# Kernel tuning notes

Hardware: AMD Instinct MI355X
Metric: run time of the kernel (lower is better)

## Reference

```python
import jax, jax.numpy as jnp
import numpy as np

DT = 0.5
DX = 0.01
MU_UP = 4e-05
PAD = 3  # 7x7 kernel // 2

_LAP = np.array([[0, 0, 0, 2, 0, 0, 0],
                 [0, 0, 0, -27, 0, 0, 0],
                 [0, 0, 0, 270, 0, 0, 0],
                 [2, -27, 270, -980, 270, -27, 2],
                 [0, 0, 0, 270, 0, 0, 0],
                 [0, 0, 0, -27, 0, 0, 0],
                 [0, 0, 0, 2, 0, 0, 0]], dtype=np.float32)
LAP_W = jnp.asarray(_LAP / (DX * DX) / 180.0)[None, None]  # [1,1,7,7]


def _laplace(x):
    # x: [B,1,H,W]; circular padding then valid conv (matches padding_mode='circular')
    xp = jnp.pad(x, ((0, 0), (0, 0), (PAD, PAD), (PAD, PAD)), mode='wrap')
    return jax.lax.conv_general_dilated(xp, LAP_W, (1, 1), 'VALID',
                                        dimension_numbers=('NCHW', 'OIHW', 'NCHW'))


def setup_inputs() -> dict:
    key = jax.random.key(0)
    ks = jax.random.split(key, 7)
    h = jax.random.uniform(ks[0], (16, 2, 1024, 1024), dtype=jnp.float32)
    CA = jax.random.uniform(ks[1], (), dtype=jnp.float32) - 0.5  # ~ -rand()+0.5
    CB = jax.random.uniform(ks[2], (), dtype=jnp.float32) - 0.5
    NA = -jax.random.uniform(ks[3], (), dtype=jnp.float32)
    NB = jax.random.uniform(ks[4], (), dtype=jnp.float32)
    f = 0.1 * jax.random.uniform(ks[5], (), dtype=jnp.float32)
    k = 0.1 * jax.random.uniform(ks[6], (), dtype=jnp.float32)
    return {"h": h, "CA": CA, "CB": CB, "NA": NA, "NB": NB, "f": f, "k": k}


def reference(h, CA, CB, NA, NB, f, k):
    mu_u = MU_UP * jax.nn.sigmoid(CA)
    mu_v = MU_UP * jax.nn.sigmoid(CB)

    def f_rhs(u, v):
        uv2 = u * v * v
        f_u = mu_u * _laplace(u) + NA * uv2 + f * (1.0 - u)
        f_v = mu_v * _laplace(v) + NB * uv2 - (k + f) * v
        return f_u, f_v

    u0 = h[:, 0:1]
    v0 = h[:, 1:2]
    k1_u, k1_v = f_rhs(u0, v0)
    k2_u, k2_v = f_rhs(u0 + k1_u * (DT / 2.0), v0 + k1_v * (DT / 2.0))
    k3_u, k3_v = f_rhs(u0 + k2_u * (DT / 2.0), v0 + k2_v * (DT / 2.0))
    k4_u, k4_v = f_rhs(u0 + k3_u * DT, v0 + k3_v * DT)
    u_next = u0 + DT * (k1_u + 2.0 * k2_u + 2.0 * k3_u + k4_u) / 6.0
    v_next = v0 + DT * (k1_v + 2.0 * k2_v + 2.0 * k3_v + k4_v) / 6.0
    return jnp.concatenate((u_next, v_next), axis=1)
```

## Files before the change

kernel.cpp:

```cpp
#include <hip/hip_runtime.h>


typedef float f2 __attribute__((ext_vector_type(2)));

#define HROWS 64
#define NT    512
#define STEPS (HROWS + 24)

#define W0 ((-980.0f / 1e-4f) / 180.0f)
#define W1 ((  270.0f / 1e-4f) / 180.0f)
#define W2 (( -27.0f / 1e-4f) / 180.0f)
#define W3 ((   2.0f / 1e-4f) / 180.0f)

__device__ __forceinline__ f2 sp(float s) { f2 r; r.x = s; r.y = s; return r; }
__device__ __forceinline__ f2 pfma(float s, f2 a, f2 c) {
    return __builtin_elementwise_fma(sp(s), a, c);
}

struct Hq { f2 m2, m1, p1, p2; };

__device__ __forceinline__ Hq rdq(const f2* __restrict__ L,
                                  int xm2, int xm1, int xp1, int xp2) {
    Hq q;
    q.m2 = L[xm2]; q.m1 = L[xm1]; q.p1 = L[xp1]; q.p2 = L[xp2];
    return q;
}

__device__ __forceinline__ void evalp(const f2* __restrict__ w, const Hq& q,
                                      f2& lap, f2& ctr)
{
    ctr = w[3];
    f2 vp = pfma(W1, w[2] + w[4], pfma(W2, w[1] + w[5], sp(W3) * (w[0] + w[6])));
    f2 m1 = __builtin_shufflevector(q.m1, ctr, 1, 2);
    f2 p1 = __builtin_shufflevector(ctr, q.p1, 1, 2);
    f2 m3 = __builtin_shufflevector(q.m2, q.m1, 1, 2);
    f2 p3 = __builtin_shufflevector(q.p1, q.p2, 1, 2);
    f2 hp = pfma(W1, m1 + p1, pfma(W2, q.m1 + q.p1, sp(W3) * (m3 + p3)));
    lap = pfma(W0, ctr, hp + vp);
}

#define SH6(A)  { A[5]=A[4]; A[4]=A[3]; A[3]=A[2]; A[2]=A[1]; A[1]=A[0]; }
#define SH7(A)  { A[6]=A[5]; A[5]=A[4]; A[4]=A[3]; A[3]=A[2]; A[2]=A[1]; A[1]=A[0]; }
#define SH10(A) { A[9]=A[8]; A[8]=A[7]; A[7]=A[6]; A[6]=A[5]; A[5]=A[4]; A[4]=A[3]; A[3]=A[2]; A[2]=A[1]; A[1]=A[0]; }

__global__ __launch_bounds__(NT, 2) void rcnn_rk4_march(
    const float* __restrict__ h,
    const float* __restrict__ pCA, const float* __restrict__ pCB,
    const float* __restrict__ pNA, const float* __restrict__ pNB,
    const float* __restrict__ pf,  const float* __restrict__ pk,
    float* __restrict__ out)
{
    __shared__ f2 Su[4][4][NT], Sv[4][4][NT];

    const int tid = threadIdx.x;
    const int Y0  = blockIdx.x * HROWS;
    const int b   = blockIdx.z;

    const float NA = pNA[0], NB = pNB[0];
    const float ff = pf[0];
    const float kpf = pk[0] + pf[0];
    const float mu_u = 4e-5f / (1.0f + expf(-pCA[0]));
    const float mu_v = 4e-5f / (1.0f + expf(-pCB[0]));

    const size_t baseU = (size_t)b * 2u * 1048576u;
    const size_t baseV = baseU + 1048576u;
    const float* hU = h + baseU + 2 * tid;
    const float* hV = h + baseV + 2 * tid;
    float* oU = out + baseU + 2 * tid;
    float* oV = out + baseV + 2 * tid;

    const int xm2 = (tid - 2) & 511;
    const int xm1 = (tid - 1) & 511;
    const int xp1 = (tid + 1) & 511;
    const int xp2 = (tid + 2) & 511;

    f2 u0u[7], u0v[7];
    f2 du[6],  dv[6];
    f2 y1u[10], y1v[10];
    f2 y2u[7],  y2v[7];
    f2 y3u[7],  y3v[7];

    const f2 z = sp(0.0f);
    #pragma unroll
    for (int j = 0; j < 7; ++j) { u0u[j]=z; u0v[j]=z; y2u[j]=z; y2v[j]=z; y3u[j]=z; y3v[j]=z; }
    #pragma unroll
    for (int j = 0; j < 6; ++j) { du[j]=z; dv[j]=z; }
    #pragma unroll
    for (int j = 0; j < 10; ++j) { y1u[j]=z; y1v[j]=z; }

    f2 p0u, p0v, p1u, p1v;
    {
        int r0 = (Y0 - 12) & 1023;
        int r1 = (Y0 - 11) & 1023;
        p0u = *(const f2*)(hU + (size_t)r0 * 1024);
        p0v = *(const f2*)(hV + (size_t)r0 * 1024);
        p1u = *(const f2*)(hU + (size_t)r1 * 1024);
        p1v = *(const f2*)(hV + (size_t)r1 * 1024);
    }

#define STEP(D1, D2, D3, D4, tt)                                              \
  {                                                                           \
    const int t_ = (tt);                                                      \
    \
    Hq q1u, q1v, q2u, q2v;                                                    \
    if (D1) { q1u = rdq(&Su[0][(t_ + 1) & 3][0], xm2, xm1, xp1, xp2);         \
              q1v = rdq(&Sv[0][(t_ + 1) & 3][0], xm2, xm1, xp1, xp2); }       \
    if (D2) { q2u = rdq(&Su[1][(t_ + 2) & 3][0], xm2, xm1, xp1, xp2);         \
              q2v = rdq(&Sv[1][(t_ + 2) & 3][0], xm2, xm1, xp1, xp2); }       \
         \
    f2 cu0 = (t_ & 1) ? p1u : p0u;                                            \
    f2 cv0 = (t_ & 1) ? p1v : p0v;                                            \
    SH6(du); SH6(dv); du[0] = u0u[6]; dv[0] = u0v[6];                         \
    SH7(u0u); SH7(u0v); u0u[0] = cu0; u0v[0] = cv0;                           \
    Su[0][t_ & 3][tid] = cu0; Sv[0][t_ & 3][tid] = cv0;                       \
            \
    {                                                                         \
      int yn = (Y0 - 10 + t_) & 1023;                                         \
      f2 au = *(const f2*)(hU + (size_t)yn * 1024);                           \
      f2 av = *(const f2*)(hV + (size_t)yn * 1024);                           \
      if (t_ & 1) { p1u = au; p1v = av; } else { p0u = au; p0v = av; }        \
    }                                                                         \
    if (D1) {                                                                 \
      f2 lU, cU1, lV, cV1;                                                    \
      evalp(u0u, q1u, lU, cU1);                                               \
      evalp(u0v, q1v, lV, cV1);                                               \
      f2 uv2 = cU1 * cV1 * cV1;                                               \
      f2 kU = pfma(mu_u, lU, pfma(NA, uv2, pfma(-ff, cU1, sp(ff))));          \
      f2 kV = pfma(mu_v, lV, pfma(NB, uv2, sp(-kpf) * cV1));                  \
      f2 nu = pfma(0.25f, kU, cU1), nv = pfma(0.25f, kV, cV1);                \
      SH10(y1u); SH10(y1v); y1u[0] = nu; y1v[0] = nv;                         \
      Su[1][(t_ + 1) & 3][tid] = nu; Sv[1][(t_ + 1) & 3][tid] = nv;           \
    }                                                                         \
    Hq q3u, q3v;                                                              \
    if (D3) { q3u = rdq(&Su[2][(t_ + 3) & 3][0], xm2, xm1, xp1, xp2);         \
              q3v = rdq(&Sv[2][(t_ + 3) & 3][0], xm2, xm1, xp1, xp2); }       \
    if (D2) {                                                                 \
      f2 lU, cU2, lV, cV2;                                                    \
      evalp(y1u, q2u, lU, cU2);                                               \
      evalp(y1v, q2v, lV, cV2);                                               \
      f2 uv2 = cU2 * cV2 * cV2;                                               \
      f2 kU = pfma(mu_u, lU, pfma(NA, uv2, pfma(-ff, cU2, sp(ff))));          \
      f2 kV = pfma(mu_v, lV, pfma(NB, uv2, sp(-kpf) * cV2));                  \
      f2 nu = pfma(0.25f, kU, u0u[6]), nv = pfma(0.25f, kV, u0v[6]);          \
      SH7(y2u); SH7(y2v); y2u[0] = nu; y2v[0] = nv;                           \
      Su[2][(t_ + 2) & 3][tid] = nu; Sv[2][(t_ + 2) & 3][tid] = nv;           \
    }                                                                         \
    Hq q4u, q4v;                                                              \
    if (D4) { q4u = rdq(&Su[3][t_ & 3][0], xm2, xm1, xp1, xp2);               \
              q4v = rdq(&Sv[3][t_ & 3][0], xm2, xm1, xp1, xp2); }             \
    if (D3) {                                                                 \
      f2 lU, cU3, lV, cV3;                                                    \
      evalp(y2u, q3u, lU, cU3);                                               \
      evalp(y2v, q3v, lV, cV3);                                               \
      f2 uv2 = cU3 * cV3 * cV3;                                               \
      f2 kU = pfma(mu_u, lU, pfma(NA, uv2, pfma(-ff, cU3, sp(ff))));          \
      f2 kV = pfma(mu_v, lV, pfma(NB, uv2, sp(-kpf) * cV3));                  \
      f2 nu = pfma(0.5f, kU, du[2]), nv = pfma(0.5f, kV, dv[2]);              \
      SH7(y3u); SH7(y3v); y3u[0] = nu; y3v[0] = nv;                           \
      Su[3][(t_ + 3) & 3][tid] = nu; Sv[3][(t_ + 3) & 3][tid] = nv;           \
    }                                                                         \
    if (D4) {                                                                 \
      f2 lU, cU4, lV, cV4;                                                    \
      evalp(y3u, q4u, lU, cU4);                                               \
      evalp(y3v, q4v, lV, cV4);                                               \
      f2 uv2 = cU4 * cV4 * cV4;                                               \
      f2 kU = pfma(mu_u, lU, pfma(NA, uv2, pfma(-ff, cU4, sp(ff))));          \
      f2 kV = pfma(mu_v, lV, pfma(NB, uv2, sp(-kpf) * cV4));                  \
      f2 aU = pfma(4.0f, y1u[9], kU);                                         \
      aU = pfma(8.0f, y2u[6], aU);                                            \
      aU = pfma(4.0f, cU4, aU);                                               \
      aU = pfma(-16.0f, du[5], aU);                                           \
      f2 aV = pfma(4.0f, y1v[9], kV);                                         \
      aV = pfma(8.0f, y2v[6], aV);                                            \
      aV = pfma(4.0f, cV4, aV);                                               \
      aV = pfma(-16.0f, dv[5], aV);                                           \
      f2 oUq = pfma(0.5f / 6.0f, aU, du[5]);                                  \
      f2 oVq = pfma(0.5f / 6.0f, aV, dv[5]);                                  \
      int yS = Y0 + t_ - 24;                                                  \
      *(f2*)(oU + (size_t)yS * 1024) = oUq;                                   \
      *(f2*)(oV + (size_t)yS * 1024) = oVq;                                   \
    }                                                                         \
    asm volatile("s_waitcnt lgkmcnt(0)" ::: "memory");                        \
    __builtin_amdgcn_s_barrier();                                             \
  }

    int t = 0;
    #pragma unroll 2
    for (; t < 6;  ++t) STEP(0, 0, 0, 0, t)
    #pragma unroll 2
    for (; t < 12; ++t) STEP(1, 0, 0, 0, t)
    #pragma unroll 2
    for (; t < 18; ++t) STEP(1, 1, 0, 0, t)
    #pragma unroll 2
    for (; t < 24; ++t) STEP(1, 1, 1, 0, t)
    #pragma unroll 4
    for (; t < STEPS; ++t) STEP(1, 1, 1, 1, t)
#undef STEP
}

extern "C" void kernel_launch(void* const* d_in, const int* in_sizes, int n_in,
                              void* d_out, int out_size, void* d_ws, size_t ws_size,
                              hipStream_t stream) {
    const float* h   = (const float*)d_in[0];
    const float* pCA = (const float*)d_in[1];
    const float* pCB = (const float*)d_in[2];
    const float* pNA = (const float*)d_in[3];
    const float* pNB = (const float*)d_in[4];
    const float* pf  = (const float*)d_in[5];
    const float* pk  = (const float*)d_in[6];
    float* outp = (float*)d_out;

    dim3 grid(1024 / HROWS, 1, 16);
    dim3 block(NT);
    rcnn_rk4_march<<<grid, block, 0, stream>>>(h, pCA, pCB, pNA, pNB, pf, pk, outp);
}
```

Measured before the change: 101.8 us.

## Replace shifting register windows with ring buffers and fold RK4 accumulation early

The per-row shifting register arrays are replaced by 8-entry ring buffers indexed by a compile-time step within an 8-way manually unrolled loop, so no register moves are needed per row. The RK4 combination is partially accumulated at stage 2 into an accumulator ring, which shortens the final output arithmetic and drops the long y1 history. Warm-up steps become runtime-guarded branches inside one unrolled loop instead of separate specialised loops. This raises code size and adds runtime branch conditions in the warm-up phase.

```diff
diff --git a/kernel.cpp b/kernel.cpp
--- a/kernel.cpp
+++ b/kernel.cpp
@@ -26,11 +26,12 @@
     return q;
 }
 
-__device__ __forceinline__ void evalp(const f2* __restrict__ w, const Hq& q,
-                                      f2& lap, f2& ctr)
+__device__ __forceinline__ void evalp7(f2 w0, f2 w1, f2 w2, f2 w3, f2 w4,
+                                       f2 w5, f2 w6, const Hq& q,
+                                       f2& lap, f2& ctr)
 {
-    ctr = w[3];
-    f2 vp = pfma(W1, w[2] + w[4], pfma(W2, w[1] + w[5], sp(W3) * (w[0] + w[6])));
+    ctr = w3;
+    f2 vp = pfma(W1, w2 + w4, pfma(W2, w1 + w5, sp(W3) * (w0 + w6)));
     f2 m1 = __builtin_shufflevector(q.m1, ctr, 1, 2);
     f2 p1 = __builtin_shufflevector(ctr, q.p1, 1, 2);
     f2 m3 = __builtin_shufflevector(q.m2, q.m1, 1, 2);
@@ -38,10 +39,6 @@
     f2 hp = pfma(W1, m1 + p1, pfma(W2, q.m1 + q.p1, sp(W3) * (m3 + p3)));
     lap = pfma(W0, ctr, hp + vp);
 }
-
-#define SH6(A)  { A[5]=A[4]; A[4]=A[3]; A[3]=A[2]; A[2]=A[1]; A[1]=A[0]; }
-#define SH7(A)  { A[6]=A[5]; A[5]=A[4]; A[4]=A[3]; A[3]=A[2]; A[2]=A[1]; A[1]=A[0]; }
-#define SH10(A) { A[9]=A[8]; A[8]=A[7]; A[7]=A[6]; A[6]=A[5]; A[5]=A[4]; A[4]=A[3]; A[3]=A[2]; A[2]=A[1]; A[1]=A[0]; }
 
 __global__ __launch_bounds__(NT, 2) void rcnn_rk4_march(
     const float* __restrict__ h,
@@ -74,108 +71,114 @@
     const int xp1 = (tid + 1) & 511;
     const int xp2 = (tid + 2) & 511;
 
-    f2 u0u[7], u0v[7];
-    f2 du[6],  dv[6];
-    f2 y1u[10], y1v[10];
-    f2 y2u[7],  y2v[7];
-    f2 y3u[7],  y3v[7];
+    f2 Uu[8], Uv[8], Du[8], Dv[8];
+    f2 Y1u[8], Y1v[8], Y2u[8], Y2v[8], Y3u[8], Y3v[8];
+    f2 ACu[8], ACv[8];
 
     const f2 z = sp(0.0f);
     #pragma unroll
-    for (int j = 0; j < 7; ++j) { u0u[j]=z; u0v[j]=z; y2u[j]=z; y2v[j]=z; y3u[j]=z; y3v[j]=z; }
-    #pragma unroll
-    for (int j = 0; j < 6; ++j) { du[j]=z; dv[j]=z; }
-    #pragma unroll
-    for (int j = 0; j < 10; ++j) { y1u[j]=z; y1v[j]=z; }
-
-    f2 p0u, p0v, p1u, p1v;
+    for (int j = 0; j < 8; ++j) {
+        Uu[j]=z; Uv[j]=z; Du[j]=z; Dv[j]=z;
+        Y1u[j]=z; Y1v[j]=z; Y2u[j]=z; Y2v[j]=z; Y3u[j]=z; Y3v[j]=z;
+        ACu[j]=z; ACv[j]=z;
+    }
+
+    f2 pAu, pAv, pBu, pBv;
     {
         int r0 = (Y0 - 12) & 1023;
         int r1 = (Y0 - 11) & 1023;
-        p0u = *(const f2*)(hU + (size_t)r0 * 1024);
-        p0v = *(const f2*)(hV + (size_t)r0 * 1024);
-        p1u = *(const f2*)(hU + (size_t)r1 * 1024);
-        p1v = *(const f2*)(hV + (size_t)r1 * 1024);
-    }
-
-#define STEP(D1, D2, D3, D4, tt)                                              \
+        pAu = *(const f2*)(hU + (size_t)r0 * 1024);
+        pAv = *(const f2*)(hV + (size_t)r0 * 1024);
+        pBu = *(const f2*)(hU + (size_t)r1 * 1024);
+        pBv = *(const f2*)(hV + (size_t)r1 * 1024);
+    }
+
+#define STEP(c, G1, G2, G3, G4)                                               \
   {                                                                           \
-    const int t_ = (tt);                                                      \
-    \
-    Hq q1u, q1v, q2u, q2v;                                                    \
-    if (D1) { q1u = rdq(&Su[0][(t_ + 1) & 3][0], xm2, xm1, xp1, xp2);         \
-              q1v = rdq(&Sv[0][(t_ + 1) & 3][0], xm2, xm1, xp1, xp2); }       \
-    if (D2) { q2u = rdq(&Su[1][(t_ + 2) & 3][0], xm2, xm1, xp1, xp2);         \
-              q2v = rdq(&Sv[1][(t_ + 2) & 3][0], xm2, xm1, xp1, xp2); }       \
-         \
-    f2 cu0 = (t_ & 1) ? p1u : p0u;                                            \
-    f2 cv0 = (t_ & 1) ? p1v : p0v;                                            \
-    SH6(du); SH6(dv); du[0] = u0u[6]; dv[0] = u0v[6];                         \
-    SH7(u0u); SH7(u0v); u0u[0] = cu0; u0v[0] = cv0;                           \
-    Su[0][t_ & 3][tid] = cu0; Sv[0][t_ & 3][tid] = cv0;                       \
-            \
+    const int t_ = tb + (c);                                                  \
+        \
+                     \
+    Hq q1u, q1v, q2u, q2v, q3u, q3v, q4u, q4v;                                \
+    if (G1) { q1u = rdq(&Su[0][((c)+1)&3][0], xm2, xm1, xp1, xp2);            \
+              q1v = rdq(&Sv[0][((c)+1)&3][0], xm2, xm1, xp1, xp2); }          \
+    if (G2) { q2u = rdq(&Su[1][((c)+2)&3][0], xm2, xm1, xp1, xp2);            \
+              q2v = rdq(&Sv[1][((c)+2)&3][0], xm2, xm1, xp1, xp2); }          \
+    if (G3) { q3u = rdq(&Su[2][((c)+3)&3][0], xm2, xm1, xp1, xp2);            \
+              q3v = rdq(&Sv[2][((c)+3)&3][0], xm2, xm1, xp1, xp2); }          \
+    if (G4) { q4u = rdq(&Su[3][(c)&3][0],     xm2, xm1, xp1, xp2);            \
+              q4v = rdq(&Sv[3][(c)&3][0],     xm2, xm1, xp1, xp2); }          \
+                    \
+    Du[(c)&7] = Uu[((c)+3)&7]; Dv[(c)&7] = Uv[((c)+3)&7];                     \
+                                             \
+    f2 cu0 = ((c) & 1) ? pBu : pAu;                                           \
+    f2 cv0 = ((c) & 1) ? pBv : pAv;                                           \
+    Uu[(c)&7] = cu0; Uv[(c)&7] = cv0;                                         \
+    Su[0][(c)&3][tid] = cu0; Sv[0][(c)&3][tid] = cv0;                         \
+                                             \
     {                                                                         \
       int yn = (Y0 - 10 + t_) & 1023;                                         \
       f2 au = *(const f2*)(hU + (size_t)yn * 1024);                           \
       f2 av = *(const f2*)(hV + (size_t)yn * 1024);                           \
-      if (t_ & 1) { p1u = au; p1v = av; } else { p0u = au; p0v = av; }        \
-    }                                                                         \
-    if (D1) {                                                                 \
-      f2 lU, cU1, lV, cV1;                                                    \
-      evalp(u0u, q1u, lU, cU1);                                               \
-      evalp(u0v, q1v, lV, cV1);                                               \
-      f2 uv2 = cU1 * cV1 * cV1;                                               \
-      f2 kU = pfma(mu_u, lU, pfma(NA, uv2, pfma(-ff, cU1, sp(ff))));          \
-      f2 kV = pfma(mu_v, lV, pfma(NB, uv2, sp(-kpf) * cV1));                  \
-      f2 nu = pfma(0.25f, kU, cU1), nv = pfma(0.25f, kV, cV1);                \
-      SH10(y1u); SH10(y1v); y1u[0] = nu; y1v[0] = nv;                         \
-      Su[1][(t_ + 1) & 3][tid] = nu; Sv[1][(t_ + 1) & 3][tid] = nv;           \
-    }                                                                         \
-    Hq q3u, q3v;                                                              \
-    if (D3) { q3u = rdq(&Su[2][(t_ + 3) & 3][0], xm2, xm1, xp1, xp2);         \
-              q3v = rdq(&Sv[2][(t_ + 3) & 3][0], xm2, xm1, xp1, xp2); }       \
-    if (D2) {                                                                 \
-      f2 lU, cU2, lV, cV2;                                                    \
-      evalp(y1u, q2u, lU, cU2);                                               \
-      evalp(y1v, q2v, lV, cV2);                                               \
-      f2 uv2 = cU2 * cV2 * cV2;                                               \
-      f2 kU = pfma(mu_u, lU, pfma(NA, uv2, pfma(-ff, cU2, sp(ff))));          \
-      f2 kV = pfma(mu_v, lV, pfma(NB, uv2, sp(-kpf) * cV2));                  \
-      f2 nu = pfma(0.25f, kU, u0u[6]), nv = pfma(0.25f, kV, u0v[6]);          \
-      SH7(y2u); SH7(y2v); y2u[0] = nu; y2v[0] = nv;                           \
-      Su[2][(t_ + 2) & 3][tid] = nu; Sv[2][(t_ + 2) & 3][tid] = nv;           \
-    }                                                                         \
-    Hq q4u, q4v;                                                              \
-    if (D4) { q4u = rdq(&Su[3][t_ & 3][0], xm2, xm1, xp1, xp2);               \
-              q4v = rdq(&Sv[3][t_ & 3][0], xm2, xm1, xp1, xp2); }             \
-    if (D3) {                                                                 \
-      f2 lU, cU3, lV, cV3;                                                    \
-      evalp(y2u, q3u, lU, cU3);                                               \
-      evalp(y2v, q3v, lV, cV3);                                               \
-      f2 uv2 = cU3 * cV3 * cV3;                                               \
-      f2 kU = pfma(mu_u, lU, pfma(NA, uv2, pfma(-ff, cU3, sp(ff))));          \
-      f2 kV = pfma(mu_v, lV, pfma(NB, uv2, sp(-kpf) * cV3));                  \
-      f2 nu = pfma(0.5f, kU, du[2]), nv = pfma(0.5f, kV, dv[2]);              \
-      SH7(y3u); SH7(y3v); y3u[0] = nu; y3v[0] = nv;                           \
-      Su[3][(t_ + 3) & 3][tid] = nu; Sv[3][(t_ + 3) & 3][tid] = nv;           \
-    }                                                                         \
-    if (D4) {                                                                 \
-      f2 lU, cU4, lV, cV4;                                                    \
-      evalp(y3u, q4u, lU, cU4);                                               \
-      evalp(y3v, q4v, lV, cV4);                                               \
-      f2 uv2 = cU4 * cV4 * cV4;                                               \
-      f2 kU = pfma(mu_u, lU, pfma(NA, uv2, pfma(-ff, cU4, sp(ff))));          \
-      f2 kV = pfma(mu_v, lV, pfma(NB, uv2, sp(-kpf) * cV4));                  \
-      f2 aU = pfma(4.0f, y1u[9], kU);                                         \
-      aU = pfma(8.0f, y2u[6], aU);                                            \
-      aU = pfma(4.0f, cU4, aU);                                               \
-      aU = pfma(-16.0f, du[5], aU);                                           \
-      f2 aV = pfma(4.0f, y1v[9], kV);                                         \
-      aV = pfma(8.0f, y2v[6], aV);                                            \
-      aV = pfma(4.0f, cV4, aV);                                               \
-      aV = pfma(-16.0f, dv[5], aV);                                           \
-      f2 oUq = pfma(0.5f / 6.0f, aU, du[5]);                                  \
-      f2 oVq = pfma(0.5f / 6.0f, aV, dv[5]);                                  \
+      if ((c) & 1) { pBu = au; pBv = av; } else { pAu = au; pAv = av; }       \
+    }                                                                         \
+    if (G1) {                                         \
+      f2 lU, cU, lV, cV;                                                      \
+      evalp7(Uu[((c)+2)&7], Uu[((c)+3)&7], Uu[((c)+4)&7], Uu[((c)+5)&7],      \
+             Uu[((c)+6)&7], Uu[((c)+7)&7], Uu[(c)&7], q1u, lU, cU);           \
+      evalp7(Uv[((c)+2)&7], Uv[((c)+3)&7], Uv[((c)+4)&7], Uv[((c)+5)&7],      \
+             Uv[((c)+6)&7], Uv[((c)+7)&7], Uv[(c)&7], q1v, lV, cV);           \
+      f2 uv2 = cU * cV * cV;                                                  \
+      f2 kU = pfma(mu_u, lU, pfma(NA, uv2, pfma(-ff, cU, sp(ff))));           \
+      f2 kV = pfma(mu_v, lV, pfma(NB, uv2, sp(-kpf) * cV));                   \
+      f2 nu = pfma(0.25f, kU, cU), nv = pfma(0.25f, kV, cV);                  \
+      Y1u[(c)&7] = nu; Y1v[(c)&7] = nv;                                       \
+      Su[1][((c)+1)&3][tid] = nu; Sv[1][((c)+1)&3][tid] = nv;                 \
+    }                                                                         \
+    if (G2) {                                         \
+      f2 lU, cU, lV, cV;                                                      \
+      evalp7(Y1u[((c)+2)&7], Y1u[((c)+3)&7], Y1u[((c)+4)&7], Y1u[((c)+5)&7],  \
+             Y1u[((c)+6)&7], Y1u[((c)+7)&7], Y1u[(c)&7], q2u, lU, cU);        \
+      evalp7(Y1v[((c)+2)&7], Y1v[((c)+3)&7], Y1v[((c)+4)&7], Y1v[((c)+5)&7],  \
+             Y1v[((c)+6)&7], Y1v[((c)+7)&7], Y1v[(c)&7], q2v, lV, cV);        \
+      f2 uv2 = cU * cV * cV;                                                  \
+      f2 kU = pfma(mu_u, lU, pfma(NA, uv2, pfma(-ff, cU, sp(ff))));           \
+      f2 kV = pfma(mu_v, lV, pfma(NB, uv2, sp(-kpf) * cV));                   \
+      f2 bu = Du[((c)+7)&7], bv = Dv[((c)+7)&7];                \
+      f2 nu = pfma(0.25f, kU, bu), nv = pfma(0.25f, kV, bv);                  \
+      Y2u[(c)&7] = nu; Y2v[(c)&7] = nv;                                       \
+      Su[2][((c)+2)&3][tid] = nu; Sv[2][((c)+2)&3][tid] = nv;                 \
+      f2 aU = pfma(4.0f, Y1u[((c)+5)&7], sp(8.0f) * nu);                      \
+      f2 aV = pfma(4.0f, Y1v[((c)+5)&7], sp(8.0f) * nv);                      \
+      ACu[(c)&7] = pfma(-4.0f, bu, aU);                                       \
+      ACv[(c)&7] = pfma(-4.0f, bv, aV);                                       \
+    }                                                                         \
+    if (G3) {                                         \
+      f2 lU, cU, lV, cV;                                                      \
+      evalp7(Y2u[((c)+2)&7], Y2u[((c)+3)&7], Y2u[((c)+4)&7], Y2u[((c)+5)&7],  \
+             Y2u[((c)+6)&7], Y2u[((c)+7)&7], Y2u[(c)&7], q3u, lU, cU);        \
+      evalp7(Y2v[((c)+2)&7], Y2v[((c)+3)&7], Y2v[((c)+4)&7], Y2v[((c)+5)&7],  \
+             Y2v[((c)+6)&7], Y2v[((c)+7)&7], Y2v[(c)&7], q3v, lV, cV);        \
+      f2 uv2 = cU * cV * cV;                                                  \
+      f2 kU = pfma(mu_u, lU, pfma(NA, uv2, pfma(-ff, cU, sp(ff))));           \
+      f2 kV = pfma(mu_v, lV, pfma(NB, uv2, sp(-kpf) * cV));                   \
+      f2 nu = pfma(0.5f, kU, Du[((c)+4)&7]);                    \
+      f2 nv = pfma(0.5f, kV, Dv[((c)+4)&7]);                                  \
+      Y3u[(c)&7] = nu; Y3v[(c)&7] = nv;                                       \
+      Su[3][((c)+3)&3][tid] = nu; Sv[3][((c)+3)&3][tid] = nv;                 \
+    }                                                                         \
+    if (G4) {                         \
+      f2 lU, cU, lV, cV;                                                      \
+      evalp7(Y3u[((c)+2)&7], Y3u[((c)+3)&7], Y3u[((c)+4)&7], Y3u[((c)+5)&7],  \
+             Y3u[((c)+6)&7], Y3u[((c)+7)&7], Y3u[(c)&7], q4u, lU, cU);        \
+      evalp7(Y3v[((c)+2)&7], Y3v[((c)+3)&7], Y3v[((c)+4)&7], Y3v[((c)+5)&7],  \
+             Y3v[((c)+6)&7], Y3v[((c)+7)&7], Y3v[(c)&7], q4v, lV, cV);        \
+      f2 uv2 = cU * cV * cV;                                                  \
+      f2 kU = pfma(mu_u, lU, pfma(NA, uv2, pfma(-ff, cU, sp(ff))));           \
+      f2 kV = pfma(mu_v, lV, pfma(NB, uv2, sp(-kpf) * cV));                   \
+      f2 sU = pfma(4.0f, cU, kU) + ACu[((c)+2)&7];             \
+      f2 sV = pfma(4.0f, cV, kV) + ACv[((c)+2)&7];                            \
+      f2 oUq = sp(1.0f / 12.0f) * sU;                                         \
+      f2 oVq = sp(1.0f / 12.0f) * sV;                                         \
       int yS = Y0 + t_ - 24;                                                  \
       *(f2*)(oU + (size_t)yS * 1024) = oUq;                                   \
       *(f2*)(oV + (size_t)yS * 1024) = oVq;                                   \
@@ -184,17 +187,20 @@
     __builtin_amdgcn_s_barrier();                                             \
   }
 
-    int t = 0;
-    #pragma unroll 2
-    for (; t < 6;  ++t) STEP(0, 0, 0, 0, t)
-    #pragma unroll 2
-    for (; t < 12; ++t) STEP(1, 0, 0, 0, t)
-    #pragma unroll 2
-    for (; t < 18; ++t) STEP(1, 1, 0, 0, t)
-    #pragma unroll 2
-    for (; t < 24; ++t) STEP(1, 1, 1, 0, t)
-    #pragma unroll 4
-    for (; t < STEPS; ++t) STEP(1, 1, 1, 1, t)
+#define STEP_W(c) STEP(c, t_ >= 6, t_ >= 12, t_ >= 18, t_ >= 24)
+#define STEP_H(c) STEP(c, 1, 1, 1, 1)
+
+    int tb = 0;
+    for (; tb < 24; tb += 8) {
+        STEP_W(0) STEP_W(1) STEP_W(2) STEP_W(3)
+        STEP_W(4) STEP_W(5) STEP_W(6) STEP_W(7)
+    }
+    for (; tb < STEPS; tb += 8) {
+        STEP_H(0) STEP_H(1) STEP_H(2) STEP_H(3)
+        STEP_H(4) STEP_H(5) STEP_H(6) STEP_H(7)
+    }
+#undef STEP_W
+#undef STEP_H
 #undef STEP
 }
 
```

Result: slower. 232.5 us (+128.4%).

## Read stage-1 horizontal neighbors from global memory instead of LDS

Applied to the files above, without the earlier changes.

Stage 1 no longer stages raw input rows in shared memory. Its horizontal neighbor reads now come straight from global memory (mostly L1/L2 hits), and the prefetch is reduced to a single row. This removes one of the four LDS ring buffers and its stores, cutting LDS footprint and traffic, which could allow more occupancy. In exchange it adds eight extra global loads per step for the stage-1 halo, and the input row is now loaded immediately before use, with less latency hiding than the old double-buffered prefetch.

```diff
diff --git a/kernel.cpp b/kernel.cpp
--- a/kernel.cpp
+++ b/kernel.cpp
@@ -50,7 +50,7 @@
     const float* __restrict__ pf,  const float* __restrict__ pk,
     float* __restrict__ out)
 {
-    __shared__ f2 Su[4][4][NT], Sv[4][4][NT];
+    __shared__ f2 Su[3][4][NT], Sv[3][4][NT];
 
     const int tid = threadIdx.x;
     const int Y0  = blockIdx.x * HROWS;
@@ -64,8 +64,10 @@
 
     const size_t baseU = (size_t)b * 2u * 1048576u;
     const size_t baseV = baseU + 1048576u;
-    const float* hU = h + baseU + 2 * tid;
-    const float* hV = h + baseV + 2 * tid;
+    const float* hU  = h + baseU;
+    const float* hV  = h + baseV;
+    const float* hUc = hU + 2 * tid;
+    const float* hVc = hV + 2 * tid;
     float* oU = out + baseU + 2 * tid;
     float* oV = out + baseV + 2 * tid;
 
@@ -88,78 +90,76 @@
     #pragma unroll
     for (int j = 0; j < 10; ++j) { y1u[j]=z; y1v[j]=z; }
 
-    f2 p0u, p0v, p1u, p1v;
+    f2 pu, pv;
     {
-        int r0 = (Y0 - 12) & 1023;
-        int r1 = (Y0 - 11) & 1023;
-        p0u = *(const f2*)(hU + (size_t)r0 * 1024);
-        p0v = *(const f2*)(hV + (size_t)r0 * 1024);
-        p1u = *(const f2*)(hU + (size_t)r1 * 1024);
-        p1v = *(const f2*)(hV + (size_t)r1 * 1024);
+        int yl = (Y0 - 12) & 1023;
+        pu = *(const f2*)(hUc + (size_t)yl * 1024);
+        pv = *(const f2*)(hVc + (size_t)yl * 1024);
     }
 
 #define STEP(D1, D2, D3, D4, tt)                                              \
   {                                                                           \
     const int t_ = (tt);                                                      \
-    \
-    Hq q1u, q1v, q2u, q2v;                                                    \
-    if (D1) { q1u = rdq(&Su[0][(t_ + 1) & 3][0], xm2, xm1, xp1, xp2);         \
-              q1v = rdq(&Sv[0][(t_ + 1) & 3][0], xm2, xm1, xp1, xp2); }       \
-    if (D2) { q2u = rdq(&Su[1][(t_ + 2) & 3][0], xm2, xm1, xp1, xp2);         \
-              q2v = rdq(&Sv[1][(t_ + 2) & 3][0], xm2, xm1, xp1, xp2); }       \
-         \
-    f2 cu0 = (t_ & 1) ? p1u : p0u;                                            \
-    f2 cv0 = (t_ & 1) ? p1v : p0v;                                            \
+     \
+    Hq q1u, q1v;                                                              \
+    if (D1) {                                                                 \
+      int ym3 = (Y0 - 15 + t_) & 1023;                                        \
+      const float* rU = hU + (size_t)ym3 * 1024;                              \
+      const float* rV = hV + (size_t)ym3 * 1024;                              \
+      q1u.m2 = *(const f2*)(rU + 2 * xm2); q1u.m1 = *(const f2*)(rU + 2 * xm1); \
+      q1u.p1 = *(const f2*)(rU + 2 * xp1); q1u.p2 = *(const f2*)(rU + 2 * xp2); \
+      q1v.m2 = *(const f2*)(rV + 2 * xm2); q1v.m1 = *(const f2*)(rV + 2 * xm1); \
+      q1v.p1 = *(const f2*)(rV + 2 * xp1); q1v.p2 = *(const f2*)(rV + 2 * xp2); \
+    }                                                                         \
+                                             \
     SH6(du); SH6(dv); du[0] = u0u[6]; dv[0] = u0v[6];                         \
-    SH7(u0u); SH7(u0v); u0u[0] = cu0; u0v[0] = cv0;                           \
-    Su[0][t_ & 3][tid] = cu0; Sv[0][t_ & 3][tid] = cv0;                       \
-            \
+    SH7(u0u); SH7(u0v); u0u[0] = pu; u0v[0] = pv;                             \
+                                             \
     {                                                                         \
-      int yn = (Y0 - 10 + t_) & 1023;                                         \
-      f2 au = *(const f2*)(hU + (size_t)yn * 1024);                           \
-      f2 av = *(const f2*)(hV + (size_t)yn * 1024);                           \
-      if (t_ & 1) { p1u = au; p1v = av; } else { p0u = au; p0v = av; }        \
-    }                                                                         \
-    if (D1) {                                                                 \
-      f2 lU, cU1, lV, cV1;                                                    \
-      evalp(u0u, q1u, lU, cU1);                                               \
-      evalp(u0v, q1v, lV, cV1);                                               \
-      f2 uv2 = cU1 * cV1 * cV1;                                               \
-      f2 kU = pfma(mu_u, lU, pfma(NA, uv2, pfma(-ff, cU1, sp(ff))));          \
-      f2 kV = pfma(mu_v, lV, pfma(NB, uv2, sp(-kpf) * cV1));                  \
-      f2 nu = pfma(0.25f, kU, cU1), nv = pfma(0.25f, kV, cV1);                \
+      int yn = (Y0 - 11 + t_) & 1023;                                         \
+      pu = *(const f2*)(hUc + (size_t)yn * 1024);                             \
+      pv = *(const f2*)(hVc + (size_t)yn * 1024);                             \
+    }                                                                         \
+    if (D1) {                                         \
+      f2 lU, cU, lV, cV;                                                      \
+      evalp(u0u, q1u, lU, cU);                                                \
+      evalp(u0v, q1v, lV, cV);                                                \
+      f2 uv2 = cU * cV * cV;                                                  \
+      f2 kU = pfma(mu_u, lU, pfma(NA, uv2, pfma(-ff, cU, sp(ff))));           \
+      f2 kV = pfma(mu_v, lV, pfma(NB, uv2, sp(-kpf) * cV));                   \
+      f2 nu = pfma(0.25f, kU, cU), nv = pfma(0.25f, kV, cV);                  \
       SH10(y1u); SH10(y1v); y1u[0] = nu; y1v[0] = nv;                         \
-      Su[1][(t_ + 1) & 3][tid] = nu; Sv[1][(t_ + 1) & 3][tid] = nv;           \
-    }                                                                         \
-    Hq q3u, q3v;                                                              \
-    if (D3) { q3u = rdq(&Su[2][(t_ + 3) & 3][0], xm2, xm1, xp1, xp2);         \
-              q3v = rdq(&Sv[2][(t_ + 3) & 3][0], xm2, xm1, xp1, xp2); }       \
-    if (D2) {                                                                 \
-      f2 lU, cU2, lV, cV2;                                                    \
-      evalp(y1u, q2u, lU, cU2);                                               \
-      evalp(y1v, q2v, lV, cV2);                                               \
-      f2 uv2 = cU2 * cV2 * cV2;                                               \
-      f2 kU = pfma(mu_u, lU, pfma(NA, uv2, pfma(-ff, cU2, sp(ff))));          \
-      f2 kV = pfma(mu_v, lV, pfma(NB, uv2, sp(-kpf) * cV2));                  \
+      Su[0][(t_ + 1) & 3][tid] = nu; Sv[0][(t_ + 1) & 3][tid] = nv;           \
+    }                                                                         \
+    if (D2) {                                         \
+      Hq q2u = rdq(&Su[0][(t_ + 2) & 3][0], xm2, xm1, xp1, xp2);              \
+      Hq q2v = rdq(&Sv[0][(t_ + 2) & 3][0], xm2, xm1, xp1, xp2);              \
+      f2 lU, cU, lV, cV;                                                      \
+      evalp(y1u, q2u, lU, cU);                                                \
+      evalp(y1v, q2v, lV, cV);                                                \
+      f2 uv2 = cU * cV * cV;                                                  \
+      f2 kU = pfma(mu_u, lU, pfma(NA, uv2, pfma(-ff, cU, sp(ff))));           \
+      f2 kV = pfma(mu_v, lV, pfma(NB, uv2, sp(-kpf) * cV));                   \
       f2 nu = pfma(0.25f, kU, u0u[6]), nv = pfma(0.25f, kV, u0v[6]);          \
       SH7(y2u); SH7(y2v); y2u[0] = nu; y2v[0] = nv;                           \
-      Su[2][(t_ + 2) & 3][tid] = nu; Sv[2][(t_ + 2) & 3][tid] = nv;           \
-    }                                                                         \
-    Hq q4u, q4v;                                                              \
-    if (D4) { q4u = rdq(&Su[3][t_ & 3][0], xm2, xm1, xp1, xp2);               \
-              q4v = rdq(&Sv[3][t_ & 3][0], xm2, xm1, xp1, xp2); }             \
-    if (D3) {                                                                 \
-      f2 lU, cU3, lV, cV3;                                                    \
-      evalp(y2u, q3u, lU, cU3);                                               \
-      evalp(y2v, q3v, lV, cV3);                                               \
-      f2 uv2 = cU3 * cV3 * cV3;                                               \
-      f2 kU = pfma(mu_u, lU, pfma(NA, uv2, pfma(-ff, cU3, sp(ff))));          \
-      f2 kV = pfma(mu_v, lV, pfma(NB, uv2, sp(-kpf) * cV3));                  \
+      Su[1][(t_ + 2) & 3][tid] = nu; Sv[1][(t_ + 2) & 3][tid] = nv;           \
+    }                                                                         \
+    if (D3) {                                         \
+      Hq q3u = rdq(&Su[1][(t_ + 3) & 3][0], xm2, xm1, xp1, xp2);              \
+      Hq q3v = rdq(&Sv[1][(t_ + 3) & 3][0], xm2, xm1, xp1, xp2);              \
+      f2 lU, cU, lV, cV;                                                      \
+      evalp(y2u, q3u, lU, cU);                                                \
+      evalp(y2v, q3v, lV, cV);                                                \
+      f2 uv2 = cU * cV * cV;                                                  \
+      f2 kU = pfma(mu_u, lU, pfma(NA, uv2, pfma(-ff, cU, sp(ff))));           \
+      f2 kV = pfma(mu_v, lV, pfma(NB, uv2, sp(-kpf) * cV));                   \
       f2 nu = pfma(0.5f, kU, du[2]), nv = pfma(0.5f, kV, dv[2]);              \
       SH7(y3u); SH7(y3v); y3u[0] = nu; y3v[0] = nv;                           \
-      Su[3][(t_ + 3) & 3][tid] = nu; Sv[3][(t_ + 3) & 3][tid] = nv;           \
-    }                                                                         \
-    if (D4) {                                                                 \
+      Su[2][(t_ + 3) & 3][tid] = nu; Sv[2][(t_ + 3) & 3][tid] = nv;           \
+    }                                                                         \
+    if (D4) {                         \
+      Hq q4u = rdq(&Su[2][t_ & 3][0], xm2, xm1, xp1, xp2);                    \
+      Hq q4v = rdq(&Sv[2][t_ & 3][0], xm2, xm1, xp1, xp2);                    \
       f2 lU, cU4, lV, cV4;                                                    \
       evalp(y3u, q4u, lU, cU4);                                               \
       evalp(y3v, q4v, lV, cV4);                                               \
@@ -174,8 +174,8 @@
       aV = pfma(8.0f, y2v[6], aV);                                            \
       aV = pfma(4.0f, cV4, aV);                                               \
       aV = pfma(-16.0f, dv[5], aV);                                           \
-      f2 oUq = pfma(0.5f / 6.0f, aU, du[5]);                                  \
-      f2 oVq = pfma(0.5f / 6.0f, aV, dv[5]);                                  \
+      f2 oUq = pfma(1.0f / 12.0f, aU, du[5]);                                 \
+      f2 oVq = pfma(1.0f / 12.0f, aV, dv[5]);                                 \
       int yS = Y0 + t_ - 24;                                                  \
       *(f2*)(oU + (size_t)yS * 1024) = oUq;                                   \
       *(f2*)(oV + (size_t)yS * 1024) = oVq;                                   \
```

After: 122.6 us. +20.5%, slower.
